# Kernel tuning notes

Measured on AMD Instinct MI355X. Metric: run time of the kernel, lower is better.

## Reference

```python
import jax, jax.numpy as jnp
import numpy as np

B, DIM1, DIM2, LATENT, T = 16, 1024, 1024, 512, 2048  # T == video_feat_dim
LN_EPS = 1e-5


def setup_inputs() -> dict:
    key = jax.random.key(0)
    ks = jax.random.split(key, 8)
    def xavier(k, shape):
        fan_out, fan_in = shape
        std = float(np.sqrt(2.0 / (fan_in + fan_out)))
        return jax.random.normal(k, shape, dtype=jnp.float32) * std
    return {
        "input1": jax.random.normal(ks[0], (B, DIM1, T), dtype=jnp.float32),
        "input2": jax.random.normal(ks[1], (B, DIM2, T), dtype=jnp.float32),
        "theta_w": xavier(ks[2], (LATENT, DIM2)),
        "theta_b": jnp.zeros((LATENT,), jnp.float32),
        "phi_w": xavier(ks[3], (LATENT, DIM1)),
        "phi_b": jnp.zeros((LATENT,), jnp.float32),
        "g_w": xavier(ks[4], (LATENT, DIM1)),
        "g_b": jnp.zeros((LATENT,), jnp.float32),
        "ln_gamma": jnp.ones((LATENT, T), jnp.float32),
        "ln_beta": jnp.zeros((LATENT, T), jnp.float32),
        "out_w": xavier(ks[5], (DIM2, LATENT)),
        "out_b": jnp.zeros((DIM2,), jnp.float32),
    }


def reference(input1, input2, theta_w, theta_b, phi_w, phi_b, g_w, g_b,
              ln_gamma, ln_beta, out_w, out_b):
    # 1x1 Conv1d == channel-wise matmul
    theta_x = jnp.einsum('ld,bdt->btl', theta_w, input2) + theta_b          # [B,T2,L]
    phi_x = jnp.einsum('ld,bdt->blt', phi_w, input1) + phi_b[:, None]       # [B,L,T1]
    scores = jnp.einsum('btl,bls->bts', theta_x, phi_x)                      # [B,T2,T1] (unscaled)
    p = jax.nn.softmax(scores, axis=-1)
    g_x = jnp.einsum('ld,bdt->btl', g_w, input1) + g_b                       # [B,T1,L]
    t_x = jnp.einsum('bts,bsl->blt', p, g_x)                                 # [B,L,T2]
    # LayerNorm over the last two dims jointly [LATENT, T]
    mu = jnp.mean(t_x, axis=(1, 2), keepdims=True)
    var = jnp.var(t_x, axis=(1, 2), keepdims=True)
    h = (t_x - mu) * jax.lax.rsqrt(var + LN_EPS) * ln_gamma + ln_beta
    h = jax.nn.relu(h)
    w_t = jnp.einsum('ol,blt->bot', out_w, h) + out_b[None, :, None]         # [B,DIM2,T2]
    return w_t + input2
```

## Files before the change

### kernel.cpp

```cpp
#include <hip/hip_runtime.h>
#include <hip/hip_bf16.h>

#define BB 16
#define D1 1024
#define D2 1024
#define LL 512
#define TT 2048
#define LN_EPS 1e-5f

typedef unsigned short u16;
typedef __attribute__((ext_vector_type(8))) _Float16 half8;
typedef __attribute__((ext_vector_type(4))) float f32x4;
typedef __attribute__((ext_vector_type(4))) unsigned int u32x4;

__device__ __forceinline__ u16 f2h(float v) {
    _Float16 h = (_Float16)v;
    return *(u16*)&h;
}
__device__ __forceinline__ float h2f(u16 u) {
    return (float)(*(const _Float16*)&u);
}

__device__ __forceinline__ void gload_lds16(const void* g, void* l) {
    __builtin_amdgcn_global_load_lds((const __attribute__((address_space(1))) void*)g,
                                     (__attribute__((address_space(3))) void*)l, 16, 0, 0);
}

__device__ __forceinline__ void stage_tile(const u16* __restrict__ g, int ldk, u16* lds, int tid) {
#pragma unroll
    for (int it = 0; it < 4; ++it) {
        int idx = it * 256 + tid;
        int m = idx >> 3, s = idx & 7;
        int gs = s ^ (m & 7);
        gload_lds16(g + (long)m * ldk + gs * 8, lds + idx * 8);
    }
}

template<int BIAS, int OMODE>
__global__ __launch_bounds__(256, 4) void nt_gemm(
    const u16* __restrict__ A, const u16* __restrict__ B,
    long sAb, long sBb, long sCb,
    int N, int Kd, int gx, int gy,
    const float* __restrict__ bias,
    void* __restrict__ out0,
    const float* __restrict__ resid, long sRb)
{
    __shared__ __align__(16) u16 smem[2 * 128 * 64];
    u16* As = smem;
    u16* Bs = smem + 128 * 64;

    const int nwg = gridDim.x;
    const int id = blockIdx.x;
    const int swz = (id & 7) * (nwg >> 3) + (id >> 3);
    const int bx = swz % gx;
    const int byz = swz / gx;
    const int by = byz % gy;
    const int b = byz / gy;

    const int tid = threadIdx.x;
    const long arow0 = (long)by * 128;
    const long brow0 = (long)bx * 128;
    const u16* Ab = A + (long)b * sAb + arow0 * Kd;
    const u16* Bb = B + (long)b * sBb + brow0 * Kd;

    const int wave = tid >> 6, lane = tid & 63;
    const int wm = (wave >> 1) * 64, wn = (wave & 1) * 64;
    const int lm = lane & 15, kg = lane >> 4;

    f32x4 acc[4][4];
#pragma unroll
    for (int i = 0; i < 4; ++i)
#pragma unroll
        for (int j = 0; j < 4; ++j) acc[i][j] = (f32x4){0.f, 0.f, 0.f, 0.f};

    for (int k0 = 0; k0 < Kd; k0 += 64) {
        stage_tile(Ab + k0, Kd, As, tid);
        stage_tile(Bb + k0, Kd, Bs, tid);
        __syncthreads();
#pragma unroll
        for (int ks = 0; ks < 2; ++ks) {
            half8 af[4], bf[4];
#pragma unroll
            for (int f = 0; f < 4; ++f) {
                int mr = wm + f * 16 + lm;
                int as_ = (ks * 4 + kg) ^ (mr & 7);
                af[f] = *(const half8*)(As + mr * 64 + as_ * 8);
                int nr = wn + f * 16 + lm;
                int bs_ = (ks * 4 + kg) ^ (nr & 7);
                bf[f] = *(const half8*)(Bs + nr * 64 + bs_ * 8);
            }
#pragma unroll
            for (int i = 0; i < 4; ++i)
#pragma unroll
                for (int j = 0; j < 4; ++j)
                    acc[i][j] = __builtin_amdgcn_mfma_f32_16x16x32_f16(af[i], bf[j], acc[i][j], 0, 0, 0);
        }
        __syncthreads();
    }

    float* Cs = (float*)smem;
#pragma unroll
    for (int p = 0; p < 2; ++p) {
        if (p) __syncthreads();
        if (wm == p * 64) {
#pragma unroll
            for (int i = 0; i < 4; ++i)
#pragma unroll
                for (int j = 0; j < 4; ++j)
#pragma unroll
                    for (int r = 0; r < 4; ++r)
                        Cs[(i * 16 + kg * 4 + r) * 128 + wn + j * 16 + lm] = acc[i][j][r];
        }
        __syncthreads();
        if (OMODE == 0 || OMODE == 3) {
#pragma unroll
            for (int rr = 0; rr < 8; ++rr) {
                int elem = rr * 256 + tid;
                int row = elem >> 5, f4 = elem & 31;
                int grow = (int)arow0 + p * 64 + row;
                int gcol = (int)brow0 + f4 * 4;
                f32x4 v = *(f32x4*)&Cs[row * 128 + f4 * 4];
                if (BIAS == 1) {
                    float bb = bias[grow];
                    v += bb;
                }
                if (BIAS == 2) {
                    f32x4 bb = *(const f32x4*)(bias + gcol);
                    v += bb;
                }
                long off = (long)b * sCb + (long)grow * N + gcol;
                if (OMODE == 3) {
                    f32x4 rv = __builtin_nontemporal_load((const f32x4*)(resid + (long)b * sRb + (long)grow * N + gcol));
                    v += rv;
                }
                __builtin_nontemporal_store(v, (f32x4*)((float*)out0 + off));
            }
        } else {
#pragma unroll
            for (int rr = 0; rr < 4; ++rr) {
                int elem = rr * 256 + tid;
                int row = elem >> 4, c8 = elem & 15;
                int grow = (int)arow0 + p * 64 + row;
                int gcol = (int)brow0 + c8 * 8;
                float vv[8];
#pragma unroll
                for (int q = 0; q < 8; ++q) vv[q] = Cs[row * 128 + c8 * 8 + q];
                if (BIAS == 1) {
                    float bb = bias[grow];
#pragma unroll
                    for (int q = 0; q < 8; ++q) vv[q] += bb;
                }
                if (BIAS == 2) {
#pragma unroll
                    for (int q = 0; q < 8; ++q) vv[q] += bias[gcol + q];
                }
                union { u16 u[8]; u32x4 v4; } pk;
#pragma unroll
                for (int q = 0; q < 8; ++q) pk.u[q] = f2h(vv[q]);
                long off = (long)b * sCb + (long)grow * N + gcol;
                __builtin_nontemporal_store(pk.v4, (u32x4*)((u16*)out0 + off));
            }
        }
    }
}

__global__ __launch_bounds__(256) void transpose_h(const float* __restrict__ in,
                                                   u16* __restrict__ o16, int D, int T) {
    __shared__ float tile[64][65];
    int b = blockIdx.z;
    const float* src = in + (long)b * D * T;
    long obase = (long)b * D * T;
    int t0 = blockIdx.x * 64, d0 = blockIdx.y * 64;
    int tx = threadIdx.x & 63, ty = threadIdx.x >> 6;
#pragma unroll
    for (int i = 0; i < 64; i += 4)
        tile[ty + i][tx] = __builtin_nontemporal_load(&src[(long)(d0 + ty + i) * T + t0 + tx]);
    __syncthreads();
#pragma unroll
    for (int i = 0; i < 64; i += 4) {
        long o = obase + (long)(t0 + ty + i) * D + d0 + tx;
        o16[o] = f2h(tile[tx][ty + i]);
    }
}

__global__ __launch_bounds__(256) void transpose_f32(const float* __restrict__ in,
                                                     float* __restrict__ out, int R, int C) {
    __shared__ float tile[64][65];
    int c0 = blockIdx.x * 64, r0 = blockIdx.y * 64;
    int tx = threadIdx.x & 63, ty = threadIdx.x >> 6;
#pragma unroll
    for (int i = 0; i < 64; i += 4)
        tile[ty + i][tx] = in[(long)(r0 + ty + i) * C + c0 + tx];
    __syncthreads();
#pragma unroll
    for (int i = 0; i < 64; i += 4)
        out[(long)(c0 + ty + i) * R + r0 + tx] = tile[tx][ty + i];
}

__global__ __launch_bounds__(256) void conv_w(const float* __restrict__ w,
                                              u16* __restrict__ h, int n) {
    int i = blockIdx.x * 256 + threadIdx.x;
    if (i < n) h[i] = f2h(w[i]);
}

__global__ __launch_bounds__(256) void softmax_rows(const float* __restrict__ S, u16* __restrict__ P) {
    long row = (long)blockIdx.z * TT + blockIdx.x;
    const float* s = S + row * TT;
    u16* p = P + row * TT;
    int tid = threadIdx.x;
    f32x4 v0 = __builtin_nontemporal_load((const f32x4*)(s + tid * 8));
    f32x4 v1 = __builtin_nontemporal_load((const f32x4*)(s + tid * 8 + 4));
    float x[8] = {v0.x, v0.y, v0.z, v0.w, v1.x, v1.y, v1.z, v1.w};
    float m = x[0];
#pragma unroll
    for (int j = 1; j < 8; ++j) m = fmaxf(m, x[j]);
#pragma unroll
    for (int off = 32; off; off >>= 1) m = fmaxf(m, __shfl_xor(m, off, 64));
    __shared__ float red[8];
    int wave = tid >> 6, lane = tid & 63;
    if (lane == 0) red[wave] = m;
    __syncthreads();
    m = fmaxf(fmaxf(red[0], red[1]), fmaxf(red[2], red[3]));
    float e[8]; float sum = 0.f;
#pragma unroll
    for (int j = 0; j < 8; ++j) { e[j] = __expf(x[j] - m); sum += e[j]; }
#pragma unroll
    for (int off = 32; off; off >>= 1) sum += __shfl_xor(sum, off, 64);
    if (lane == 0) red[4 + wave] = sum;
    __syncthreads();
    sum = red[4] + red[5] + red[6] + red[7];
    float inv = 1.f / sum;
    union { u16 u[8]; u32x4 v4; } pk;
#pragma unroll
    for (int j = 0; j < 8; ++j) pk.u[j] = f2h(e[j] * inv);
    *(u32x4*)(p + tid * 8) = pk.v4;
}

__global__ void zero32(float* p) { p[threadIdx.x] = 0.f; }

__global__ __launch_bounds__(256) void ln_partial(const u16* __restrict__ TXp, float* __restrict__ sums) {
    int b = blockIdx.z;
    const u16* x = TXp + (long)b * (LL * TT) + (long)blockIdx.x * 32768;
    int tid = threadIdx.x;
    float s = 0.f, sq = 0.f;
#pragma unroll 4
    for (int j = 0; j < 16; ++j) {
        u32x4 v = *(const u32x4*)(x + (j * 256 + tid) * 8);
        unsigned w[4] = {v.x, v.y, v.z, v.w};
#pragma unroll
        for (int q = 0; q < 4; ++q) {
            float a = h2f((u16)(w[q] & 0xffff));
            float c = h2f((u16)(w[q] >> 16));
            s += a + c;
            sq += a * a + c * c;
        }
    }
#pragma unroll
    for (int off = 32; off; off >>= 1) { s += __shfl_xor(s, off, 64); sq += __shfl_xor(sq, off, 64); }
    __shared__ float rs[8];
    int wave = tid >> 6, lane = tid & 63;
    if (lane == 0) { rs[wave] = s; rs[4 + wave] = sq; }
    __syncthreads();
    if (tid == 0) {
        atomicAdd(&sums[b * 2], rs[0] + rs[1] + rs[2] + rs[3]);
        atomicAdd(&sums[b * 2 + 1], rs[4] + rs[5] + rs[6] + rs[7]);
    }
}

__global__ __launch_bounds__(256) void ln_apply(const u16* __restrict__ TXp, const float* __restrict__ sums,
                                                const float* __restrict__ gT, const float* __restrict__ bT,
                                                u16* __restrict__ H) {
    int b = blockIdx.z;
    const float n = (float)(LL * TT);
    float mu = sums[b * 2] / n;
    float var = sums[b * 2 + 1] / n - mu * mu;
    float rstd = rsqrtf(var + LN_EPS);
    long base = (long)b * (LL * TT);
    long idx = ((long)blockIdx.x * 256 + threadIdx.x) * 8;
    u32x4 xv = *(const u32x4*)(TXp + base + idx);
    unsigned w[4] = {xv.x, xv.y, xv.z, xv.w};
    f32x4 g0 = *(const f32x4*)(gT + idx);
    f32x4 g1 = *(const f32x4*)(gT + idx + 4);
    f32x4 b0 = *(const f32x4*)(bT + idx);
    f32x4 b1 = *(const f32x4*)(bT + idx + 4);
    float g[8] = {g0.x, g0.y, g0.z, g0.w, g1.x, g1.y, g1.z, g1.w};
    float be[8] = {b0.x, b0.y, b0.z, b0.w, b1.x, b1.y, b1.z, b1.w};
    union { u16 u[8]; u32x4 v; } pk;
#pragma unroll
    for (int q = 0; q < 4; ++q) {
        float a = h2f((u16)(w[q] & 0xffff));
        float c = h2f((u16)(w[q] >> 16));
        float oa = fmaxf((a - mu) * rstd * g[q * 2] + be[q * 2], 0.f);
        float oc = fmaxf((c - mu) * rstd * g[q * 2 + 1] + be[q * 2 + 1], 0.f);
        pk.u[q * 2] = f2h(oa);
        pk.u[q * 2 + 1] = f2h(oc);
    }
    *(u32x4*)(H + base + idx) = pk.v;
}

extern "C" void kernel_launch(void* const* d_in, const int* in_sizes, int n_in,
                              void* d_out, int out_size, void* d_ws, size_t ws_size,
                              hipStream_t stream) {
    const float* input1  = (const float*)d_in[0];
    const float* input2  = (const float*)d_in[1];
    const float* theta_w = (const float*)d_in[2];
    const float* theta_b = (const float*)d_in[3];
    const float* phi_w   = (const float*)d_in[4];
    const float* phi_b   = (const float*)d_in[5];
    const float* g_w     = (const float*)d_in[6];
    const float* g_b     = (const float*)d_in[7];
    const float* ln_gamma= (const float*)d_in[8];
    const float* ln_beta = (const float*)d_in[9];
    const float* out_w   = (const float*)d_in[10];
    const float* out_b   = (const float*)d_in[11];
    float* out = (float*)d_out;

    char* ws = (char*)d_ws;
    const size_t MB = 1ull << 20;
    u16*  Xt     = (u16*)(ws + 0);
    float* scores= (float*)(ws + 0);
    u16*  pmat   = (u16*)(ws + 64 * MB);
    u16*  Qf     = (u16*)(ws + 96 * MB);
    u16*  Kf     = (u16*)(ws + 128 * MB);
    u16*  Vt     = (u16*)(ws + 160 * MB);
    u16*  TX     = (u16*)(ws + 192 * MB);
    u16*  H      = (u16*)(ws + 224 * MB);
    u16*  thw    = (u16*)(ws + 256 * MB);
    u16*  phw    = (u16*)(ws + 257 * MB);
    u16*  gww    = (u16*)(ws + 258 * MB);
    u16*  oww    = (u16*)(ws + 259 * MB);
    float* gammaT= (float*)(ws + 260 * MB);
    float* betaT = (float*)(ws + 264 * MB);
    float* sums  = (float*)(ws + 268 * MB);

    dim3 blk(256);

    conv_w<<<dim3((LL * D2 + 255) / 256), blk, 0, stream>>>(theta_w, thw, LL * D2);
    conv_w<<<dim3((LL * D1 + 255) / 256), blk, 0, stream>>>(phi_w, phw, LL * D1);
    conv_w<<<dim3((LL * D1 + 255) / 256), blk, 0, stream>>>(g_w, gww, LL * D1);
    conv_w<<<dim3((D2 * LL + 255) / 256), blk, 0, stream>>>(out_w, oww, D2 * LL);
    transpose_f32<<<dim3(TT / 64, LL / 64, 1), blk, 0, stream>>>(ln_gamma, gammaT, LL, TT);
    transpose_f32<<<dim3(TT / 64, LL / 64, 1), blk, 0, stream>>>(ln_beta, betaT, LL, TT);

    transpose_h<<<dim3(TT / 64, D2 / 64, BB), blk, 0, stream>>>(input2, Xt, D2, TT);
    nt_gemm<2, 1><<<dim3((LL / 128) * (TT / 128) * BB), blk, 0, stream>>>(
        Xt, thw, (long)TT * D2, 0, (long)TT * LL, LL, D2, LL / 128, TT / 128,
        theta_b, Qf, nullptr, 0);

    transpose_h<<<dim3(TT / 64, D1 / 64, BB), blk, 0, stream>>>(input1, Xt, D1, TT);
    nt_gemm<2, 1><<<dim3((LL / 128) * (TT / 128) * BB), blk, 0, stream>>>(
        Xt, phw, (long)TT * D1, 0, (long)TT * LL, LL, D1, LL / 128, TT / 128,
        phi_b, Kf, nullptr, 0);
    nt_gemm<1, 1><<<dim3((TT / 128) * (LL / 128) * BB), blk, 0, stream>>>(
        gww, Xt, 0, (long)TT * D1, (long)LL * TT, TT, D1, TT / 128, LL / 128,
        g_b, Vt, nullptr, 0);

    for (int c = 0; c < 4; ++c) {
        long qoff = (long)c * 4 * TT * LL;
        nt_gemm<0, 0><<<dim3((TT / 128) * (TT / 128) * 4), blk, 0, stream>>>(
            Qf + qoff, Kf + qoff, (long)TT * LL, (long)TT * LL, (long)TT * TT,
            TT, LL, TT / 128, TT / 128, nullptr, scores, nullptr, 0);
        softmax_rows<<<dim3(TT, 1, 4), blk, 0, stream>>>(scores, pmat);
        nt_gemm<0, 1><<<dim3((LL / 128) * (TT / 128) * 4), blk, 0, stream>>>(
            pmat, Vt + (long)c * 4 * LL * TT, (long)TT * TT, (long)LL * TT, (long)TT * LL,
            LL, TT, LL / 128, TT / 128, nullptr, TX + qoff, nullptr, 0);
    }

    zero32<<<dim3(1), dim3(32), 0, stream>>>(sums);
    ln_partial<<<dim3(32, 1, BB), blk, 0, stream>>>(TX, sums);
    ln_apply<<<dim3(512, 1, BB), blk, 0, stream>>>(TX, sums, gammaT, betaT, H);

    nt_gemm<1, 3><<<dim3((TT / 128) * (D2 / 128) * BB), blk, 0, stream>>>(
        oww, H, 0, (long)TT * LL, (long)D2 * TT, TT, LL, TT / 128, D2 / 128,
        out_b, out, input2, (long)D2 * TT);
}
```

Baseline: 660.5 us.

## Use 256x256 double-buffered GEMM tiles and batch the P·V GEMM

The NT GEMM moves from 128x128 tiles with 256 threads to 256x256 tiles with 512 threads. It double-buffers LDS (128KB) with direct global-to-LDS loads, partial vmcnt waits, and s_setprio around the MFMA blocks. The epilogue uses an XOR-swizzled LDS layout to cut bank conflicts. The P·V GEMM now runs once over all batches after the softmax loop, which grows the workspace so pmat can hold all 16 probability matrices. Larger tiles raise data reuse but lower occupancy and the number of workgroups per launch.

```diff
diff --git a/kernel.cpp b/kernel.cpp
--- a/kernel.cpp
+++ b/kernel.cpp
@@ -26,18 +26,13 @@
                                      (__attribute__((address_space(3))) void*)l, 16, 0, 0);
 }
 
-__device__ __forceinline__ void stage_tile(const u16* __restrict__ g, int ldk, u16* lds, int tid) {
-#pragma unroll
-    for (int it = 0; it < 4; ++it) {
-        int idx = it * 256 + tid;
-        int m = idx >> 3, s = idx & 7;
-        int gs = s ^ (m & 7);
-        gload_lds16(g + (long)m * ldk + gs * 8, lds + idx * 8);
-    }
+#define MEMFENCE asm volatile("" ::: "memory")
+__device__ __forceinline__ void block_barrier() {
+    MEMFENCE; __builtin_amdgcn_s_barrier(); MEMFENCE;
 }
 
 template<int BIAS, int OMODE>
-__global__ __launch_bounds__(256, 4) void nt_gemm(
+__global__ __launch_bounds__(512, 2) void nt_gemm(
     const u16* __restrict__ A, const u16* __restrict__ B,
     long sAb, long sBb, long sCb,
     int N, int Kd, int gx, int gy,
@@ -45,9 +40,7 @@
     void* __restrict__ out0,
     const float* __restrict__ resid, long sRb)
 {
-    __shared__ __align__(16) u16 smem[2 * 128 * 64];
-    u16* As = smem;
-    u16* Bs = smem + 128 * 64;
+    __shared__ __align__(16) u16 smem[65536];
 
     const int nwg = gridDim.x;
     const int id = blockIdx.x;
@@ -58,93 +51,135 @@
     const int b = byz / gy;
 
     const int tid = threadIdx.x;
-    const long arow0 = (long)by * 128;
-    const long brow0 = (long)bx * 128;
+    const long arow0 = (long)by * 256;
+    const long brow0 = (long)bx * 256;
     const u16* Ab = A + (long)b * sAb + arow0 * Kd;
     const u16* Bb = B + (long)b * sBb + brow0 * Kd;
 
     const int wave = tid >> 6, lane = tid & 63;
-    const int wm = (wave >> 1) * 64, wn = (wave & 1) * 64;
+    const int wm = (wave >> 2) * 128, wn = (wave & 3) * 64;
     const int lm = lane & 15, kg = lane >> 4;
 
-    f32x4 acc[4][4];
-#pragma unroll
-    for (int i = 0; i < 4; ++i)
+    const int m0 = tid >> 3, s0 = tid & 7;
+    const int nt = Kd >> 6;
+
+    auto STAGE = [&](int buf, long k0) {
+        u16* Ad = smem + buf * 32768;
+        u16* Bd = smem + buf * 32768 + 16384;
+#pragma unroll
+        for (int call = 0; call < 4; ++call) {
+            int m = call * 64 + m0;
+            int gs = s0 ^ (m & 7);
+            gload_lds16(Ab + k0 + (long)m * Kd + gs * 8, Ad + (call * 512 + tid) * 8);
+        }
+#pragma unroll
+        for (int call = 0; call < 4; ++call) {
+            int m = call * 64 + m0;
+            int gs = s0 ^ (m & 7);
+            gload_lds16(Bb + k0 + (long)m * Kd + gs * 8, Bd + (call * 512 + tid) * 8);
+        }
+    };
+
+    f32x4 acc[8][4];
+#pragma unroll
+    for (int i = 0; i < 8; ++i)
 #pragma unroll
         for (int j = 0; j < 4; ++j) acc[i][j] = (f32x4){0.f, 0.f, 0.f, 0.f};
 
-    for (int k0 = 0; k0 < Kd; k0 += 64) {
-        stage_tile(Ab + k0, Kd, As, tid);
-        stage_tile(Bb + k0, Kd, Bs, tid);
+    STAGE(0, 0);
+    if (nt > 1) STAGE(1, 64);
+
+    for (int t = 0; t < nt; ++t) {
+        const int cur = t & 1;
+        if (t + 1 < nt) { asm volatile("s_waitcnt vmcnt(8)" ::: "memory"); }
+        else           { asm volatile("s_waitcnt vmcnt(0)" ::: "memory"); }
+        block_barrier();
+
+        const u16* Ac = smem + cur * 32768;
+        const u16* Bc = smem + cur * 32768 + 16384;
+
+        half8 bf[4][2];
+#pragma unroll
+        for (int f = 0; f < 4; ++f)
+#pragma unroll
+            for (int kf = 0; kf < 2; ++kf) {
+                int nr = wn + f * 16 + lm;
+                int ss = (kf * 4 + kg) ^ (nr & 7);
+                bf[f][kf] = *(const half8*)(Bc + nr * 64 + ss * 8);
+            }
+#pragma unroll
+        for (int mh = 0; mh < 2; ++mh) {
+            half8 af[4][2];
+#pragma unroll
+            for (int f = 0; f < 4; ++f)
+#pragma unroll
+                for (int kf = 0; kf < 2; ++kf) {
+                    int mr = wm + mh * 64 + f * 16 + lm;
+                    int ss = (kf * 4 + kg) ^ (mr & 7);
+                    af[f][kf] = *(const half8*)(Ac + mr * 64 + ss * 8);
+                }
+            __builtin_amdgcn_s_setprio(1);
+#pragma unroll
+            for (int f = 0; f < 4; ++f)
+#pragma unroll
+                for (int j = 0; j < 4; ++j)
+#pragma unroll
+                    for (int kf = 0; kf < 2; ++kf)
+                        acc[mh * 4 + f][j] = __builtin_amdgcn_mfma_f32_16x16x32_f16(
+                            af[f][kf], bf[j][kf], acc[mh * 4 + f][j], 0, 0, 0);
+            __builtin_amdgcn_s_setprio(0);
+        }
+        block_barrier();
+        if (t + 2 < nt) STAGE(cur, (long)(t + 2) * 64);
+    }
+
+    float* Cs = (float*)smem;
+#pragma unroll
+    for (int p = 0; p < 2; ++p) {
         __syncthreads();
-#pragma unroll
-        for (int ks = 0; ks < 2; ++ks) {
-            half8 af[4], bf[4];
-#pragma unroll
-            for (int f = 0; f < 4; ++f) {
-                int mr = wm + f * 16 + lm;
-                int as_ = (ks * 4 + kg) ^ (mr & 7);
-                af[f] = *(const half8*)(As + mr * 64 + as_ * 8);
-                int nr = wn + f * 16 + lm;
-                int bs_ = (ks * 4 + kg) ^ (nr & 7);
-                bf[f] = *(const half8*)(Bs + nr * 64 + bs_ * 8);
-            }
-#pragma unroll
-            for (int i = 0; i < 4; ++i)
+        if (wm == p * 128) {
+#pragma unroll
+            for (int i = 0; i < 8; ++i)
 #pragma unroll
                 for (int j = 0; j < 4; ++j)
-                    acc[i][j] = __builtin_amdgcn_mfma_f32_16x16x32_f16(af[i], bf[j], acc[i][j], 0, 0, 0);
-        }
-        __syncthreads();
-    }
-
-    float* Cs = (float*)smem;
-#pragma unroll
-    for (int p = 0; p < 2; ++p) {
-        if (p) __syncthreads();
-        if (wm == p * 64) {
-#pragma unroll
-            for (int i = 0; i < 4; ++i)
-#pragma unroll
-                for (int j = 0; j < 4; ++j)
-#pragma unroll
-                    for (int r = 0; r < 4; ++r)
-                        Cs[(i * 16 + kg * 4 + r) * 128 + wn + j * 16 + lm] = acc[i][j][r];
+#pragma unroll
+                    for (int r = 0; r < 4; ++r) {
+                        int row = i * 16 + kg * 4 + r;
+                        int col = wn + j * 16 + lm;
+                        Cs[row * 256 + (col ^ ((row & 7) << 2))] = acc[i][j][r];
+                    }
         }
         __syncthreads();
         if (OMODE == 0 || OMODE == 3) {
 #pragma unroll
-            for (int rr = 0; rr < 8; ++rr) {
-                int elem = rr * 256 + tid;
-                int row = elem >> 5, f4 = elem & 31;
-                int grow = (int)arow0 + p * 64 + row;
-                int gcol = (int)brow0 + f4 * 4;
-                f32x4 v = *(f32x4*)&Cs[row * 128 + f4 * 4];
-                if (BIAS == 1) {
-                    float bb = bias[grow];
-                    v += bb;
-                }
-                if (BIAS == 2) {
-                    f32x4 bb = *(const f32x4*)(bias + gcol);
-                    v += bb;
-                }
+            for (int it = 0; it < 16; ++it) {
+                int elem = it * 512 + tid;
+                int row = elem >> 6, c4 = elem & 63;
+                int grow = (int)arow0 + p * 128 + row;
+                int gcol = (int)brow0 + c4 * 4;
+                f32x4 v = *(const f32x4*)&Cs[row * 256 + ((c4 ^ (row & 7)) << 2)];
+                if (BIAS == 1) v += bias[grow];
+                if (BIAS == 2) v += *(const f32x4*)(bias + gcol);
                 long off = (long)b * sCb + (long)grow * N + gcol;
                 if (OMODE == 3) {
-                    f32x4 rv = __builtin_nontemporal_load((const f32x4*)(resid + (long)b * sRb + (long)grow * N + gcol));
+                    f32x4 rv = __builtin_nontemporal_load(
+                        (const f32x4*)(resid + (long)b * sRb + (long)grow * N + gcol));
                     v += rv;
                 }
                 __builtin_nontemporal_store(v, (f32x4*)((float*)out0 + off));
             }
         } else {
 #pragma unroll
-            for (int rr = 0; rr < 4; ++rr) {
-                int elem = rr * 256 + tid;
-                int row = elem >> 4, c8 = elem & 15;
-                int grow = (int)arow0 + p * 64 + row;
+            for (int it = 0; it < 8; ++it) {
+                int elem = it * 512 + tid;
+                int row = elem >> 5, c8 = elem & 31;
+                int grow = (int)arow0 + p * 128 + row;
                 int gcol = (int)brow0 + c8 * 8;
-                float vv[8];
-#pragma unroll
-                for (int q = 0; q < 8; ++q) vv[q] = Cs[row * 128 + c8 * 8 + q];
+                int g0 = (c8 * 2) ^ (row & 7);
+                int g1 = (c8 * 2 + 1) ^ (row & 7);
+                f32x4 u0 = *(const f32x4*)&Cs[row * 256 + g0 * 4];
+                f32x4 u1 = *(const f32x4*)&Cs[row * 256 + g1 * 4];
+                float vv[8] = {u0.x, u0.y, u0.z, u0.w, u1.x, u1.y, u1.z, u1.w};
                 if (BIAS == 1) {
                     float bb = bias[grow];
 #pragma unroll
@@ -320,20 +355,20 @@
     u16*  Xt     = (u16*)(ws + 0);
     float* scores= (float*)(ws + 0);
     u16*  pmat   = (u16*)(ws + 64 * MB);
-    u16*  Qf     = (u16*)(ws + 96 * MB);
-    u16*  Kf     = (u16*)(ws + 128 * MB);
-    u16*  Vt     = (u16*)(ws + 160 * MB);
-    u16*  TX     = (u16*)(ws + 192 * MB);
-    u16*  H      = (u16*)(ws + 224 * MB);
-    u16*  thw    = (u16*)(ws + 256 * MB);
-    u16*  phw    = (u16*)(ws + 257 * MB);
-    u16*  gww    = (u16*)(ws + 258 * MB);
-    u16*  oww    = (u16*)(ws + 259 * MB);
-    float* gammaT= (float*)(ws + 260 * MB);
-    float* betaT = (float*)(ws + 264 * MB);
-    float* sums  = (float*)(ws + 268 * MB);
-
-    dim3 blk(256);
+    u16*  Qf     = (u16*)(ws + 192 * MB);
+    u16*  Kf     = (u16*)(ws + 224 * MB);
+    u16*  Vt     = (u16*)(ws + 256 * MB);
+    u16*  TX     = (u16*)(ws + 288 * MB);
+    u16*  H      = (u16*)(ws + 320 * MB);
+    u16*  thw    = (u16*)(ws + 352 * MB);
+    u16*  phw    = (u16*)(ws + 353 * MB);
+    u16*  gww    = (u16*)(ws + 354 * MB);
+    u16*  oww    = (u16*)(ws + 355 * MB);
+    float* gammaT= (float*)(ws + 356 * MB);
+    float* betaT = (float*)(ws + 360 * MB);
+    float* sums  = (float*)(ws + 364 * MB);
+
+    dim3 blk(256), blk5(512);
 
     conv_w<<<dim3((LL * D2 + 255) / 256), blk, 0, stream>>>(theta_w, thw, LL * D2);
     conv_w<<<dim3((LL * D1 + 255) / 256), blk, 0, stream>>>(phi_w, phw, LL * D1);
@@ -343,34 +378,34 @@
     transpose_f32<<<dim3(TT / 64, LL / 64, 1), blk, 0, stream>>>(ln_beta, betaT, LL, TT);
 
     transpose_h<<<dim3(TT / 64, D2 / 64, BB), blk, 0, stream>>>(input2, Xt, D2, TT);
-    nt_gemm<2, 1><<<dim3((LL / 128) * (TT / 128) * BB), blk, 0, stream>>>(
-        Xt, thw, (long)TT * D2, 0, (long)TT * LL, LL, D2, LL / 128, TT / 128,
+    nt_gemm<2, 1><<<dim3((LL / 256) * (TT / 256) * BB), blk5, 0, stream>>>(
+        Xt, thw, (long)TT * D2, 0, (long)TT * LL, LL, D2, LL / 256, TT / 256,
         theta_b, Qf, nullptr, 0);
 
     transpose_h<<<dim3(TT / 64, D1 / 64, BB), blk, 0, stream>>>(input1, Xt, D1, TT);
-    nt_gemm<2, 1><<<dim3((LL / 128) * (TT / 128) * BB), blk, 0, stream>>>(
-        Xt, phw, (long)TT * D1, 0, (long)TT * LL, LL, D1, LL / 128, TT / 128,
+    nt_gemm<2, 1><<<dim3((LL / 256) * (TT / 256) * BB), blk5, 0, stream>>>(
+        Xt, phw, (long)TT * D1, 0, (long)TT * LL, LL, D1, LL / 256, TT / 256,
         phi_b, Kf, nullptr, 0);
-    nt_gemm<1, 1><<<dim3((TT / 128) * (LL / 128) * BB), blk, 0, stream>>>(
-        gww, Xt, 0, (long)TT * D1, (long)LL * TT, TT, D1, TT / 128, LL / 128,
+    nt_gemm<1, 1><<<dim3((TT / 256) * (LL / 256) * BB), blk5, 0, stream>>>(
+        gww, Xt, 0, (long)TT * D1, (long)LL * TT, TT, D1, TT / 256, LL / 256,
         g_b, Vt, nullptr, 0);
 
     for (int c = 0; c < 4; ++c) {
         long qoff = (long)c * 4 * TT * LL;
-        nt_gemm<0, 0><<<dim3((TT / 128) * (TT / 128) * 4), blk, 0, stream>>>(
+        nt_gemm<0, 0><<<dim3((TT / 256) * (TT / 256) * 4), blk5, 0, stream>>>(
             Qf + qoff, Kf + qoff, (long)TT * LL, (long)TT * LL, (long)TT * TT,
-            TT, LL, TT / 128, TT / 128, nullptr, scores, nullptr, 0);
-        softmax_rows<<<dim3(TT, 1, 4), blk, 0, stream>>>(scores, pmat);
-        nt_gemm<0, 1><<<dim3((LL / 128) * (TT / 128) * 4), blk, 0, stream>>>(
-            pmat, Vt + (long)c * 4 * LL * TT, (long)TT * TT, (long)LL * TT, (long)TT * LL,
-            LL, TT, LL / 128, TT / 128, nullptr, TX + qoff, nullptr, 0);
-    }
+            TT, LL, TT / 256, TT / 256, nullptr, scores, nullptr, 0);
+        softmax_rows<<<dim3(TT, 1, 4), blk, 0, stream>>>(scores, pmat + (long)c * 4 * TT * TT);
+    }
+    nt_gemm<0, 1><<<dim3((LL / 256) * (TT / 256) * BB), blk5, 0, stream>>>(
+        pmat, Vt, (long)TT * TT, (long)LL * TT, (long)TT * LL,
+        LL, TT, LL / 256, TT / 256, nullptr, TX, nullptr, 0);
 
     zero32<<<dim3(1), dim3(32), 0, stream>>>(sums);
     ln_partial<<<dim3(32, 1, BB), blk, 0, stream>>>(TX, sums);
     ln_apply<<<dim3(512, 1, BB), blk, 0, stream>>>(TX, sums, gammaT, betaT, H);
 
-    nt_gemm<1, 3><<<dim3((TT / 128) * (D2 / 128) * BB), blk, 0, stream>>>(
-        oww, H, 0, (long)TT * LL, (long)D2 * TT, TT, LL, TT / 128, D2 / 128,
+    nt_gemm<1, 3><<<dim3((TT / 256) * (D2 / 256) * BB), blk5, 0, stream>>>(
+        oww, H, 0, (long)TT * LL, (long)D2 * TT, TT, LL, TT / 256, D2 / 256,
         out_b, out, input2, (long)D2 * TT);
 }
```

Measured after the change: 585.6 us. 11.3% less time.
